# Kernel optimization log

Hardware: AMD Instinct MI355X
Metric: run time of the kernel (lower is better)

## Reference

```python
import jax, jax.numpy as jnp
import numpy as np

POOLED = 7      # pooled_size
KSIZE = 2       # kernel_size (max-pool window & stride)
CROP = POOLED * KSIZE  # crop_and_resize crop_size = 14


def setup_inputs() -> dict:
    key = jax.random.key(0)
    k1, k2 = jax.random.split(key)
    feature_maps = jax.random.normal(k1, (2, 50, 50, 512), dtype=jnp.float32)
    # normalized boxes in [x1, y1, x2, y2] order (the layer swaps to y1,x1,y2,x2);
    # tf.image.crop_and_resize handles arbitrary (even inverted) boxes, so raw
    # uniforms are valid inputs.
    rois = jax.random.uniform(k2, (2, 128, 4), dtype=jnp.float32)
    return {"feature_maps": feature_maps, "rois": rois}


def _roi_pool(feature_maps, rois):
    B, H, W, C = feature_maps.shape
    R = rois.shape[1]
    N = B * R
    # [x1,y1,x2,y2] -> [y1,x1,y2,x2] as in the layer
    boxes = rois.reshape(N, 4)[:, jnp.array([1, 0, 3, 2])]
    y1, x1, y2, x2 = boxes[:, 0], boxes[:, 1], boxes[:, 2], boxes[:, 3]
    bidx = jnp.repeat(jnp.arange(B), R)  # box_indices, [N]

    # tf.image.crop_and_resize sample grid (crop_size > 1 branch)
    i = jnp.arange(CROP, dtype=feature_maps.dtype)
    ys = y1[:, None] * (H - 1) + i[None, :] * ((y2 - y1)[:, None] * (H - 1) / (CROP - 1))  # [N,S]
    xs = x1[:, None] * (W - 1) + i[None, :] * ((x2 - x1)[:, None] * (W - 1) / (CROP - 1))  # [N,S]
    valid_y = (ys >= 0) & (ys <= H - 1)
    valid_x = (xs >= 0) & (xs <= W - 1)

    y0f = jnp.floor(ys)
    x0f = jnp.floor(xs)
    wy = (ys - y0f)[:, :, None, None]   # [N,S,1,1]
    wx = (xs - x0f)[:, None, :, None]   # [N,1,S,1]
    y0i = jnp.clip(y0f.astype(jnp.int32), 0, H - 1)
    y1i = jnp.clip(y0i + 1, 0, H - 1)
    x0i = jnp.clip(x0f.astype(jnp.int32), 0, W - 1)
    x1i = jnpp = None
    x1i = jnp.clip(x0i + 1, 0, W - 1)

    # gather the two bilinear rows per sample line: [N, S, W, C]
    rows0 = feature_maps[bidx[:, None], y0i]
    rows1 = feature_maps[bidx[:, None], y1i]
    rows = rows0 + (rows1 - rows0) * wy  # lerp in y

    # gather the two columns and lerp in x: [N, S, S, C]
    v0 = jnp.take_along_axis(rows, x0i[:, None, :, None], axis=2)
    v1 = jnp.take_along_axis(rows, x1i[:, None, :, None], axis=2)
    crops = v0 + (v1 - v0) * wx

    # out-of-range samples -> extrapolation_value = 0 (TF default)
    valid = valid_y[:, :, None, None] & valid_x[:, None, :, None]
    crops = jnp.where(valid, crops, jnp.zeros((), crops.dtype))

    # 2x2/stride-2 max pool -> [N, POOLED, POOLED, C]
    pooled = crops.reshape(N, POOLED, KSIZE, POOLED, KSIZE, C).max(axis=(2, 4))
    return pooled


def reference(feature_maps, rois):
    # flatten=False, keep_batch_dim=False -> [batch*num_rois, pooled, pooled, C]
    return _roi_pool(feature_maps, rois)
```

## Files before the change

### kernel.cpp

```cpp
#include <hip/hip_runtime.h>
#include <hip/hip_fp16.h>


constexpr int H = 50, W = 50, C = 512;
constexpr int POOLEDX = 7, KSIZE = 2, CROP = 14;
constexpr int RPB = 128;
constexpr int PIX = POOLEDX * POOLEDX;
constexpr int NROI = 2 * RPB;
constexpr int NTASK = NROI * PIX;
constexpr int NELEM = 2 * H * W * C;
constexpr int NBLK  = NTASK / 4;
constexpr int NXCD  = 8;
constexpr int CHUNK = NBLK / NXCD;

typedef _Float16 h8 __attribute__((ext_vector_type(8)));
typedef float    f4 __attribute__((ext_vector_type(4)));

__global__ __launch_bounds__(256) void cvt_kernel(
    const float* __restrict__ in, __half* __restrict__ out)
{
    const int i = (blockIdx.x * 256 + threadIdx.x) * 8;
    const f4* in4 = reinterpret_cast<const f4*>(in + i);
    const f4 a = __builtin_nontemporal_load(in4);
    const f4 b = __builtin_nontemporal_load(in4 + 1);
    _Float16 h[8];
    h[0] = (_Float16)a[0]; h[1] = (_Float16)a[1];
    h[2] = (_Float16)a[2]; h[3] = (_Float16)a[3];
    h[4] = (_Float16)b[0]; h[5] = (_Float16)b[1];
    h[6] = (_Float16)b[2]; h[7] = (_Float16)b[3];
    *reinterpret_cast<f4*>(out + i) = *reinterpret_cast<const f4*>(h);
}

__global__ __launch_bounds__(256, 4) void roi_pool_kernel(
    const __half* __restrict__ fmh,
    const float* __restrict__ rois,
    float* __restrict__ out)
{
    const int wv   = __builtin_amdgcn_readfirstlane((int)(threadIdx.x >> 6));
    const int lane = threadIdx.x & 63;

    const int bid  = blockIdx.x;
    const int swz  = (bid & (NXCD - 1)) * CHUNK + (bid >> 3);
    const int task = swz * 4 + wv;

    const int n  = task / PIX;
    const int k  = task - n * PIX;
    const int ph = k / POOLEDX;
    const int pw = k - ph * POOLEDX;
    const int bat = n / RPB;

    const float rx1 = rois[n*4+0], ry1 = rois[n*4+1];
    const float rx2 = rois[n*4+2], ry2 = rois[n*4+3];
    const float ybase = ry1 * (float)(H - 1);
    const float xbase = rx1 * (float)(W - 1);
    const float ystep = ((ry2 - ry1) * (float)(H - 1)) / (float)(CROP - 1);
    const float xstep = ((rx2 - rx1) * (float)(W - 1)) / (float)(CROP - 1);

    int   x0i[KSIZE], x1i[KSIZE];
    float wx[KSIZE];
    bool  vx[KSIZE];
    #pragma unroll
    for (int kx = 0; kx < KSIZE; ++kx) {
        const float xs = xbase + (float)(pw * KSIZE + kx) * xstep;
        vx[kx] = (xs >= 0.0f) && (xs <= (float)(W - 1));
        const float xf = floorf(xs);
        wx[kx] = xs - xf;
        int xi = (int)xf; xi = min(max(xi, 0), W - 1);
        x0i[kx] = xi;
        x1i[kx] = min(xi + 1, W - 1);
    }

    const __half* base = fmh + (long)bat * (H * W) * C + lane * 8;

    h8 acc;
    #pragma unroll
    for (int c = 0; c < 8; ++c) acc[c] = (_Float16)(-60000.0f);

    #pragma unroll
    for (int ky = 0; ky < KSIZE; ++ky) {
        const float ys = ybase + (float)(ph * KSIZE + ky) * ystep;
        const bool  vy = (ys >= 0.0f) && (ys <= (float)(H - 1));
        const float yf = floorf(ys);
        const float wy = ys - yf;
        int y0 = (int)yf; y0 = min(max(y0, 0), H - 1);
        const int y1 = min(y0 + 1, H - 1);

        #pragma unroll
        for (int kx = 0; kx < KSIZE; ++kx) {
            const h8 t00 = *reinterpret_cast<const h8*>(base + (long)(y0 * W + x0i[kx]) * C);
            const h8 t01 = *reinterpret_cast<const h8*>(base + (long)(y0 * W + x1i[kx]) * C);
            const h8 t10 = *reinterpret_cast<const h8*>(base + (long)(y1 * W + x0i[kx]) * C);
            const h8 t11 = *reinterpret_cast<const h8*>(base + (long)(y1 * W + x1i[kx]) * C);

            const float wxk = wx[kx];
            const _Float16 w00 = (_Float16)((1.0f - wy) * (1.0f - wxk));
            const _Float16 w01 = (_Float16)((1.0f - wy) * wxk);
            const _Float16 w10 = (_Float16)(wy * (1.0f - wxk));
            const _Float16 w11 = (_Float16)(wy * wxk);

            h8 v = t00 * w00 + t01 * w01 + t10 * w10 + t11 * w11;

            if (!(vx[kx] && vy)) {
                #pragma unroll
                for (int c = 0; c < 8; ++c) v[c] = (_Float16)0.0f;
            }

#if __has_builtin(__builtin_elementwise_max)
            acc = __builtin_elementwise_max(acc, v);
#else
            #pragma unroll
            for (int c = 0; c < 8; ++c) acc[c] = acc[c] > v[c] ? acc[c] : v[c];
#endif
        }
    }

    f4 o0, o1;
    o0[0] = (float)acc[0]; o0[1] = (float)acc[1]; o0[2] = (float)acc[2]; o0[3] = (float)acc[3];
    o1[0] = (float)acc[4]; o1[1] = (float)acc[5]; o1[2] = (float)acc[6]; o1[3] = (float)acc[7];
    f4* out4 = reinterpret_cast<f4*>(out) + (long)task * (C / 4) + lane * 2;
    __builtin_nontemporal_store(o0, out4);
    __builtin_nontemporal_store(o1, out4 + 1);
}

extern "C" void kernel_launch(void* const* d_in, const int* in_sizes, int n_in,
                              void* d_out, int out_size, void* d_ws, size_t ws_size,
                              hipStream_t stream) {
    const float* fm   = (const float*)d_in[0];
    const float* rois = (const float*)d_in[1];
    float* out  = (float*)d_out;
    __half* fmh = (__half*)d_ws;

    cvt_kernel<<<NELEM / (256 * 8), 256, 0, stream>>>(fm, fmh);
    roi_pool_kernel<<<NBLK, 256, 0, stream>>>(fmh, rois, out);
}
```

Measured before the change: 78.83 us.

## Make ROI pool kernel persistent with double-buffered register prefetch of gathers

Replaces the one-task-per-wave grid with a persistent grid of 512 blocks in which each wave processes seven tasks strided across all waves. Two register buffers alternate so that the sixteen gathered h8 loads for the next task are issued before the current task is blended, overlapping memory latency with compute. The validity masks are folded into the bilinear weights instead of a branch. In exchange the XCD-aware block swizzle is dropped, register pressure rises (launch bounds lowered to 2 blocks per CU), and the tail uses clamped duplicate loads plus a guarded store.

```diff
diff --git a/kernel.cpp b/kernel.cpp
--- a/kernel.cpp
+++ b/kernel.cpp
@@ -9,9 +9,9 @@
 constexpr int NROI = 2 * RPB;
 constexpr int NTASK = NROI * PIX;
 constexpr int NELEM = 2 * H * W * C;
-constexpr int NBLK  = NTASK / 4;
-constexpr int NXCD  = 8;
-constexpr int CHUNK = NBLK / NXCD;
+constexpr int PBLK  = 512;
+constexpr int NWAVE = PBLK * 4;
+constexpr int NITER = 7;
 
 typedef _Float16 h8 __attribute__((ext_vector_type(8)));
 typedef float    f4 __attribute__((ext_vector_type(4)));
@@ -31,95 +31,129 @@
     *reinterpret_cast<f4*>(out + i) = *reinterpret_cast<const f4*>(h);
 }
 
-__global__ __launch_bounds__(256, 4) void roi_pool_kernel(
+#define DECLBUF(S)                                                           \
+    h8 S##q0, S##q1, S##q2,  S##q3,  S##q4,  S##q5,  S##q6,  S##q7,          \
+       S##q8, S##q9, S##q10, S##q11, S##q12, S##q13, S##q14, S##q15;         \
+    float S##wx0, S##wx1, S##wy0, S##wy1, S##m00, S##m01, S##m10, S##m11;    \
+    int S##task;
+
+#define TFETCH(S, T)                                                         \
+  {                                                                          \
+    S##task = (T);                                                           \
+    const int tc  = min(S##task, NTASK - 1);                                 \
+    const int n   = tc / PIX;                                                \
+    const int kk  = tc - n * PIX;                                            \
+    const int ph  = kk / POOLEDX;                                            \
+    const int pw  = kk - ph * POOLEDX;                                       \
+    const int boff = (n / RPB) * (H * W * C);                                \
+    const float rx1 = rois[n*4+0], ry1 = rois[n*4+1];                        \
+    const float rx2 = rois[n*4+2], ry2 = rois[n*4+3];                        \
+    const float ybase = ry1 * (float)(H-1);                                  \
+    const float xbase = rx1 * (float)(W-1);                                  \
+    const float ystep = ((ry2-ry1)*(float)(H-1)) * (1.0f/(float)(CROP-1));   \
+    const float xstep = ((rx2-rx1)*(float)(W-1)) * (1.0f/(float)(CROP-1));   \
+    const float xs0 = xbase + (float)(pw*KSIZE+0)*xstep;                     \
+    const float xs1 = xbase + (float)(pw*KSIZE+1)*xstep;                     \
+    const float ys0 = ybase + (float)(ph*KSIZE+0)*ystep;                     \
+    const float ys1 = ybase + (float)(ph*KSIZE+1)*ystep;                     \
+    const float mx0 = (xs0>=0.0f && xs0<=(float)(W-1)) ? 1.0f : 0.0f;        \
+    const float mx1 = (xs1>=0.0f && xs1<=(float)(W-1)) ? 1.0f : 0.0f;        \
+    const float my0 = (ys0>=0.0f && ys0<=(float)(H-1)) ? 1.0f : 0.0f;        \
+    const float my1 = (ys1>=0.0f && ys1<=(float)(H-1)) ? 1.0f : 0.0f;        \
+    const float xf0 = floorf(xs0), xf1 = floorf(xs1);                        \
+    const float yf0 = floorf(ys0), yf1 = floorf(ys1);                        \
+    S##wx0 = xs0 - xf0; S##wx1 = xs1 - xf1;                                  \
+    S##wy0 = ys0 - yf0; S##wy1 = ys1 - yf1;                                  \
+    S##m00 = mx0*my0; S##m01 = mx1*my0;                                      \
+    S##m10 = mx0*my1; S##m11 = mx1*my1;                                      \
+    int xi0 = (int)xf0; xi0 = min(max(xi0,0),W-1);                           \
+    int xi1 = (int)xf1; xi1 = min(max(xi1,0),W-1);                           \
+    int yi0 = (int)yf0; yi0 = min(max(yi0,0),H-1);                           \
+    int yi1 = (int)yf1; yi1 = min(max(yi1,0),H-1);                           \
+    const int cx00 = __builtin_amdgcn_readfirstlane(xi0) * C;                \
+    const int cx10 = __builtin_amdgcn_readfirstlane(min(xi0+1,W-1)) * C;     \
+    const int cx01 = __builtin_amdgcn_readfirstlane(xi1) * C;                \
+    const int cx11 = __builtin_amdgcn_readfirstlane(min(xi1+1,W-1)) * C;     \
+    const int ry00 = __builtin_amdgcn_readfirstlane(yi0) * (W*C);            \
+    const int ry10 = __builtin_amdgcn_readfirstlane(min(yi0+1,H-1)) * (W*C); \
+    const int ry01 = __builtin_amdgcn_readfirstlane(yi1) * (W*C);            \
+    const int ry11 = __builtin_amdgcn_readfirstlane(min(yi1+1,H-1)) * (W*C); \
+    const __half* bb = lanebase + boff;                                      \
+    S##q0  = *reinterpret_cast<const h8*>(bb + ry00 + cx00);                 \
+    S##q1  = *reinterpret_cast<const h8*>(bb + ry00 + cx10);                 \
+    S##q2  = *reinterpret_cast<const h8*>(bb + ry10 + cx00);                 \
+    S##q3  = *reinterpret_cast<const h8*>(bb + ry10 + cx10);                 \
+    S##q4  = *reinterpret_cast<const h8*>(bb + ry00 + cx01);                 \
+    S##q5  = *reinterpret_cast<const h8*>(bb + ry00 + cx11);                 \
+    S##q6  = *reinterpret_cast<const h8*>(bb + ry10 + cx01);                 \
+    S##q7  = *reinterpret_cast<const h8*>(bb + ry10 + cx11);                 \
+    S##q8  = *reinterpret_cast<const h8*>(bb + ry01 + cx00);                 \
+    S##q9  = *reinterpret_cast<const h8*>(bb + ry01 + cx10);                 \
+    S##q10 = *reinterpret_cast<const h8*>(bb + ry11 + cx00);                 \
+    S##q11 = *reinterpret_cast<const h8*>(bb + ry11 + cx10);                 \
+    S##q12 = *reinterpret_cast<const h8*>(bb + ry01 + cx01);                 \
+    S##q13 = *reinterpret_cast<const h8*>(bb + ry01 + cx11);                 \
+    S##q14 = *reinterpret_cast<const h8*>(bb + ry11 + cx01);                 \
+    S##q15 = *reinterpret_cast<const h8*>(bb + ry11 + cx11);                 \
+  }
+
+#define TGROUP(S, QA, QB, QC, QD, WY, WX, M)                                 \
+  { const float wy = S##WY, wx = S##WX, m = S##M;                            \
+    const _Float16 w00 = (_Float16)((1.0f-wy)*(1.0f-wx)*m);                  \
+    const _Float16 w01 = (_Float16)((1.0f-wy)*wx*m);                         \
+    const _Float16 w10 = (_Float16)(wy*(1.0f-wx)*m);                         \
+    const _Float16 w11 = (_Float16)(wy*wx*m);                                \
+    const h8 v = S##QA*w00 + S##QB*w01 + S##QC*w10 + S##QD*w11;              \
+    acc = __builtin_elementwise_max(acc, v); }
+
+#define TCONSUME(S)                                                          \
+  {                                                                          \
+    h8 acc;                                                                  \
+    _Pragma("unroll")                                                        \
+    for (int c = 0; c < 8; ++c) acc[c] = (_Float16)(-60000.0f);              \
+    TGROUP(S, q0,  q1,  q2,  q3,  wy0, wx0, m00)                             \
+    TGROUP(S, q4,  q5,  q6,  q7,  wy0, wx1, m01)                             \
+    TGROUP(S, q8,  q9,  q10, q11, wy1, wx0, m10)                             \
+    TGROUP(S, q12, q13, q14, q15, wy1, wx1, m11)                             \
+    if (S##task < NTASK) {                                                   \
+      f4 o0, o1;                                                             \
+      o0[0]=(float)acc[0]; o0[1]=(float)acc[1];                              \
+      o0[2]=(float)acc[2]; o0[3]=(float)acc[3];                              \
+      o1[0]=(float)acc[4]; o1[1]=(float)acc[5];                              \
+      o1[2]=(float)acc[6]; o1[3]=(float)acc[7];                              \
+      f4* out4 = reinterpret_cast<f4*>(out) + (long)S##task*(C/4) + lane*2;  \
+      __builtin_nontemporal_store(o0, out4);                                 \
+      __builtin_nontemporal_store(o1, out4 + 1);                             \
+    }                                                                        \
+  }
+
+__global__ __launch_bounds__(256, 2) void roi_pool_kernel(
     const __half* __restrict__ fmh,
     const float* __restrict__ rois,
     float* __restrict__ out)
 {
     const int wv   = __builtin_amdgcn_readfirstlane((int)(threadIdx.x >> 6));
     const int lane = threadIdx.x & 63;
+    const int wave = blockIdx.x * 4 + wv;
+    const __half* lanebase = fmh + lane * 8;
 
-    const int bid  = blockIdx.x;
-    const int swz  = (bid & (NXCD - 1)) * CHUNK + (bid >> 3);
-    const int task = swz * 4 + wv;
+    DECLBUF(A)
+    DECLBUF(B)
 
-    const int n  = task / PIX;
-    const int k  = task - n * PIX;
-    const int ph = k / POOLEDX;
-    const int pw = k - ph * POOLEDX;
-    const int bat = n / RPB;
-
-    const float rx1 = rois[n*4+0], ry1 = rois[n*4+1];
-    const float rx2 = rois[n*4+2], ry2 = rois[n*4+3];
-    const float ybase = ry1 * (float)(H - 1);
-    const float xbase = rx1 * (float)(W - 1);
-    const float ystep = ((ry2 - ry1) * (float)(H - 1)) / (float)(CROP - 1);
-    const float xstep = ((rx2 - rx1) * (float)(W - 1)) / (float)(CROP - 1);
-
-    int   x0i[KSIZE], x1i[KSIZE];
-    float wx[KSIZE];
-    bool  vx[KSIZE];
-    #pragma unroll
-    for (int kx = 0; kx < KSIZE; ++kx) {
-        const float xs = xbase + (float)(pw * KSIZE + kx) * xstep;
-        vx[kx] = (xs >= 0.0f) && (xs <= (float)(W - 1));
-        const float xf = floorf(xs);
-        wx[kx] = xs - xf;
-        int xi = (int)xf; xi = min(max(xi, 0), W - 1);
-        x0i[kx] = xi;
-        x1i[kx] = min(xi + 1, W - 1);
-    }
-
-    const __half* base = fmh + (long)bat * (H * W) * C + lane * 8;
-
-    h8 acc;
-    #pragma unroll
-    for (int c = 0; c < 8; ++c) acc[c] = (_Float16)(-60000.0f);
-
-    #pragma unroll
-    for (int ky = 0; ky < KSIZE; ++ky) {
-        const float ys = ybase + (float)(ph * KSIZE + ky) * ystep;
-        const bool  vy = (ys >= 0.0f) && (ys <= (float)(H - 1));
-        const float yf = floorf(ys);
-        const float wy = ys - yf;
-        int y0 = (int)yf; y0 = min(max(y0, 0), H - 1);
-        const int y1 = min(y0 + 1, H - 1);
-
-        #pragma unroll
-        for (int kx = 0; kx < KSIZE; ++kx) {
-            const h8 t00 = *reinterpret_cast<const h8*>(base + (long)(y0 * W + x0i[kx]) * C);
-            const h8 t01 = *reinterpret_cast<const h8*>(base + (long)(y0 * W + x1i[kx]) * C);
-            const h8 t10 = *reinterpret_cast<const h8*>(base + (long)(y1 * W + x0i[kx]) * C);
-            const h8 t11 = *reinterpret_cast<const h8*>(base + (long)(y1 * W + x1i[kx]) * C);
-
-            const float wxk = wx[kx];
-            const _Float16 w00 = (_Float16)((1.0f - wy) * (1.0f - wxk));
-            const _Float16 w01 = (_Float16)((1.0f - wy) * wxk);
-            const _Float16 w10 = (_Float16)(wy * (1.0f - wxk));
-            const _Float16 w11 = (_Float16)(wy * wxk);
-
-            h8 v = t00 * w00 + t01 * w01 + t10 * w10 + t11 * w11;
-
-            if (!(vx[kx] && vy)) {
-                #pragma unroll
-                for (int c = 0; c < 8; ++c) v[c] = (_Float16)0.0f;
-            }
-
-#if __has_builtin(__builtin_elementwise_max)
-            acc = __builtin_elementwise_max(acc, v);
-#else
-            #pragma unroll
-            for (int c = 0; c < 8; ++c) acc[c] = acc[c] > v[c] ? acc[c] : v[c];
-#endif
-        }
-    }
-
-    f4 o0, o1;
-    o0[0] = (float)acc[0]; o0[1] = (float)acc[1]; o0[2] = (float)acc[2]; o0[3] = (float)acc[3];
-    o1[0] = (float)acc[4]; o1[1] = (float)acc[5]; o1[2] = (float)acc[6]; o1[3] = (float)acc[7];
-    f4* out4 = reinterpret_cast<f4*>(out) + (long)task * (C / 4) + lane * 2;
-    __builtin_nontemporal_store(o0, out4);
-    __builtin_nontemporal_store(o1, out4 + 1);
+    TFETCH(A, wave)
+    TFETCH(B, wave + 1*NWAVE)
+    TCONSUME(A)
+    TFETCH(A, wave + 2*NWAVE)
+    TCONSUME(B)
+    TFETCH(B, wave + 3*NWAVE)
+    TCONSUME(A)
+    TFETCH(A, wave + 4*NWAVE)
+    TCONSUME(B)
+    TFETCH(B, wave + 5*NWAVE)
+    TCONSUME(A)
+    TFETCH(A, wave + 6*NWAVE)
+    TCONSUME(B)
+    TCONSUME(A)
 }
 
 extern "C" void kernel_launch(void* const* d_in, const int* in_sizes, int n_in,
@@ -131,5 +165,5 @@
     __half* fmh = (__half*)d_ws;
 
     cvt_kernel<<<NELEM / (256 * 8), 256, 0, stream>>>(fm, fmh);
-    roi_pool_kernel<<<NBLK, 256, 0, stream>>>(fmh, rois, out);
+    roi_pool_kernel<<<PBLK, 256, 0, stream>>>(fmh, rois, out);
 }
```

Result: no change. 80.09 us (+1.6%).
